# Kernel optimization log

Measured on AMD Instinct MI355X. Metric: run time of the kernel, lower is better.

Reference implementation:

```python
import jax, jax.numpy as jnp
import numpy as np

DIM = 3
LAM = 500.0  # Poisson rate from __init__
LOG2PI = float(np.log(2.0 * np.pi))
JITTER = 1e-6


def setup_inputs() -> dict:
    key = jax.random.key(0)
    ks = jax.random.split(key, 12)
    Lang, A, K, N = 500, 32, 64, 512
    colors = jax.random.normal(ks[0], (Lang, K, DIM), dtype=jnp.float32) * 2.0
    # each alignment is K DISTINCT prototype indices (DPP submatrix must be non-singular)
    u = jax.random.uniform(ks[1], (Lang, A, N))
    alignments = jnp.argsort(u, axis=-1)[..., :K].astype(jnp.int32)
    mus = jax.random.normal(ks[2], (N, DIM), dtype=jnp.float32)
    fk_w1 = jax.random.normal(ks[3], (DIM, DIM), dtype=jnp.float32) * 0.3
    fk_b1 = jax.random.normal(ks[4], (DIM,), dtype=jnp.float32) * 0.1
    fk_w2 = jax.random.normal(ks[5], (1, DIM), dtype=jnp.float32) * 0.3
    fk_b2 = jax.random.normal(ks[6], (1,), dtype=jnp.float32) * 0.1
    df_w1 = jnp.eye(DIM, dtype=jnp.float32) + 0.1 * jax.random.normal(ks[7], (DIM, DIM), dtype=jnp.float32)
    df_b1 = jax.random.normal(ks[8], (DIM,), dtype=jnp.float32) * 0.1
    # last layer initialized to identity in the original module; perturb slightly, keep invertible
    df_w2 = jnp.eye(DIM, dtype=jnp.float32) + 0.05 * jax.random.normal(ks[9], (DIM, DIM), dtype=jnp.float32)
    df_b2 = jax.random.normal(ks[10], (DIM,), dtype=jnp.float32) * 0.1
    return {"colors": colors, "alignments": alignments, "mus": mus,
            "fk_w1": fk_w1, "fk_b1": fk_b1, "fk_w2": fk_w2, "fk_b2": fk_b2,
            "df_w1": df_w1, "df_b1": df_b1, "df_w2": df_w2, "df_b2": df_b2}


def reference(colors, alignments, mus, fk_w1, fk_b1, fk_w2, fk_b2, df_w1, df_b1, df_w2, df_b2):
    N = mus.shape[0]
    K = alignments.shape[-1]

    # step1: Poisson(lambda).log_prob(N)
    Nf = jnp.float32(N)
    step1 = Nf * jnp.log(LAM) - LAM - jax.scipy.special.gammaln(Nf + 1.0)

    # step2: standard MVN prior on prototypes, summed
    step2 = jnp.sum(-0.5 * jnp.sum(mus * mus, axis=-1) - 0.5 * DIM * LOG2PI)

    # L-ensemble: quality (focalization MLP) x RBF diversity
    h = jnp.tanh(mus @ fk_w1.T + fk_b1)            # [N, 3]
    logq = (h @ fk_w2.T + fk_b2)[:, 0]             # [N]
    q = jnp.exp(logq)
    d2 = jnp.sum((mus[:, None, :] - mus[None, :, :]) ** 2, axis=-1)  # [N, N]
    S = jnp.exp(-0.5 * d2)
    L = q[:, None] * S * q[None, :]                # [N, N]
    logdet_LI = jnp.linalg.slogdet(L + jnp.eye(N, dtype=L.dtype))[1]

    # step3: DPP log-prob per alignment: logdet(L_A) - logdet(L + I)
    sub = L[alignments[..., :, None], alignments[..., None, :]]       # [Lang, A, K, K]
    sub = sub + JITTER * jnp.eye(K, dtype=L.dtype)
    step3 = jnp.linalg.slogdet(sub)[1] - logdet_LI                    # [Lang, A]

    # step4: chromes = inverse diffeomorphism of colors (Linear-Tanh-Linear inverted)
    w2_inv = jnp.linalg.inv(df_w2)
    w1_inv = jnp.linalg.inv(df_w1)
    z2 = (colors - df_b2) @ w2_inv.T
    z1 = jnp.arctanh(jnp.clip(z2, -1.0 + 1e-6, 1.0 - 1e-6))
    chromes = (z1 - df_b1) @ w1_inv.T                                 # [Lang, K, 3]

    chromemes = mus[alignments]                                       # [Lang, A, K, 3]
    diff = chromes[:, None, :, :] - chromemes                         # [Lang, A, K, 3]
    step4 = jnp.sum(-0.5 * jnp.sum(diff * diff, axis=-1) - 0.5 * DIM * LOG2PI, axis=-1)  # [Lang, A]

    # per-language logsumexp over alignments, summed over languages
    step34 = jnp.sum(jax.scipy.special.logsumexp(step3 + step4, axis=-1))

    return -(step1 + step2 + step34)
```

## Files before the change

### kernel.cpp

```cpp
#include <hip/hip_runtime.h>
#include <math.h>

#define LOG2PI_F 1.8378770664093453f

#define WS_Q    0
#define WS_SCAL 512
#define WS_M    544
#define WS_CHR  (544 + 512*512)
#define WS_S34  (WS_CHR + 96000)
#define WS_BAR  (WS_S34 + 16000)

#define CHOL_BLOCKS 16

__device__ inline void inv3(const float* w, float* out){
  float a=w[0],b=w[1],c=w[2],d=w[3],e=w[4],f=w[5],g=w[6],h=w[7],i=w[8];
  float A = e*i - f*h;
  float B = -(d*i - f*g);
  float C = d*h - e*g;
  float det = a*A + b*B + c*C;
  float id = 1.0f/det;
  out[0]=A*id;            out[1]=-(b*i - c*h)*id; out[2]=(b*f - c*e)*id;
  out[3]=B*id;            out[4]=(a*i - c*g)*id;  out[5]=-(a*f - c*d)*id;
  out[6]=C*id;            out[7]=-(a*h - b*g)*id; out[8]=(a*e - b*d)*id;
}

__device__ inline void wave_lds_sync(){
  asm volatile("s_waitcnt lgkmcnt(0)" ::: "memory");
}

__device__ inline float rdlane(float v, int l){
  return __int_as_float(__builtin_amdgcn_readlane(__float_as_int(v), l));
}

__device__ inline void gbar(float* ws){
  __syncthreads();
  if (threadIdx.x == 0){
    int* cnt = (int*)(ws + WS_BAR);
    int* gen = (int*)(ws + WS_BAR) + 1;
    int g = __hip_atomic_load(gen, __ATOMIC_RELAXED, __HIP_MEMORY_SCOPE_AGENT);
    int a = __hip_atomic_fetch_add(cnt, 1, __ATOMIC_ACQ_REL, __HIP_MEMORY_SCOPE_AGENT);
    if (a == CHOL_BLOCKS - 1){
      __hip_atomic_store(cnt, 0, __ATOMIC_RELAXED, __HIP_MEMORY_SCOPE_AGENT);
      __hip_atomic_store(gen, g + 1, __ATOMIC_RELEASE, __HIP_MEMORY_SCOPE_AGENT);
    } else {
      while (__hip_atomic_load(gen, __ATOMIC_RELAXED, __HIP_MEMORY_SCOPE_AGENT) == g){
        __builtin_amdgcn_s_sleep(1);
      }
      (void)__hip_atomic_load(gen, __ATOMIC_ACQUIRE, __HIP_MEMORY_SCOPE_AGENT);
    }
  }
  __syncthreads();
}

__global__ __launch_bounds__(512) void k_prep(const float* __restrict__ mus,
    const float* __restrict__ fkw1, const float* __restrict__ fkb1,
    const float* __restrict__ fkw2, const float* __restrict__ fkb2,
    const float* __restrict__ dfw1, const float* __restrict__ dfw2,
    float* ws){
  int t = threadIdx.x;
  __shared__ float red[512];
  float m0 = mus[t*3+0], m1 = mus[t*3+1], m2 = mus[t*3+2];
  float h0 = tanhf(fkw1[0]*m0 + fkw1[1]*m1 + fkw1[2]*m2 + fkb1[0]);
  float h1 = tanhf(fkw1[3]*m0 + fkw1[4]*m1 + fkw1[5]*m2 + fkb1[1]);
  float h2 = tanhf(fkw1[6]*m0 + fkw1[7]*m1 + fkw1[8]*m2 + fkb1[2]);
  float logq = fkw2[0]*h0 + fkw2[1]*h1 + fkw2[2]*h2 + fkb2[0];
  ws[WS_Q + t] = expf(logq);
  red[t] = -0.5f*(m0*m0 + m1*m1 + m2*m2);
  __syncthreads();
  for (int s = 256; s; s >>= 1){ if (t < s) red[t] += red[t+s]; __syncthreads(); }
  if (t == 0){
    ws[WS_SCAL+1] = red[0] - 512.0f*1.5f*LOG2PI_F;
    ws[WS_SCAL+0] = 512.0f*logf(500.0f) - 500.0f - lgammaf(513.0f);
    inv3(dfw1, ws + WS_SCAL + 3);
    inv3(dfw2, ws + WS_SCAL + 12);
    ((int*)(ws + WS_BAR))[0] = 0;
    ((int*)(ws + WS_BAR))[1] = 0;
  }
}

__global__ __launch_bounds__(256) void k_cl(const float* __restrict__ colors,
    const float* __restrict__ dfb1, const float* __restrict__ dfb2,
    const float* __restrict__ mus, float* ws){
  const int b = blockIdx.x;
  if (b < 125){
    int id = b*256 + threadIdx.x;
    const float* w1i = ws + WS_SCAL + 3;
    const float* w2i = ws + WS_SCAL + 12;
    float c0 = colors[id*3+0] - dfb2[0];
    float c1 = colors[id*3+1] - dfb2[1];
    float c2 = colors[id*3+2] - dfb2[2];
    float z0 = w2i[0]*c0 + w2i[1]*c1 + w2i[2]*c2;
    float z1 = w2i[3]*c0 + w2i[4]*c1 + w2i[5]*c2;
    float z2 = w2i[6]*c0 + w2i[7]*c1 + w2i[8]*c2;
    const float lo = -1.0f + 1e-6f, hi = 1.0f - 1e-6f;
    z0 = atanhf(fminf(fmaxf(z0, lo), hi)) - dfb1[0];
    z1 = atanhf(fminf(fmaxf(z1, lo), hi)) - dfb1[1];
    z2 = atanhf(fminf(fmaxf(z2, lo), hi)) - dfb1[2];
    ws[WS_CHR + id*3+0] = w1i[0]*z0 + w1i[1]*z1 + w1i[2]*z2;
    ws[WS_CHR + id*3+1] = w1i[3]*z0 + w1i[4]*z1 + w1i[5]*z2;
    ws[WS_CHR + id*3+2] = w1i[6]*z0 + w1i[7]*z1 + w1i[8]*z2;
  } else {
    int id = (b - 125)*256 + threadIdx.x;
    int i = id >> 9, j = id & 511;
    float dx = mus[i*3+0]-mus[j*3+0];
    float dy = mus[i*3+1]-mus[j*3+1];
    float dz = mus[i*3+2]-mus[j*3+2];
    float d2 = dx*dx + dy*dy + dz*dz;
    float v = ws[WS_Q+i]*ws[WS_Q+j]*expf(-0.5f*d2);
    if (i == j) v += 1.0f;
    ws[WS_M + id] = v;
  }
}

__global__ __launch_bounds__(512) void k_fused(const int* __restrict__ align,
    const float* __restrict__ mus, float* ws){
  __shared__ __align__(16) float smem[16384];

  if (blockIdx.x < CHOL_BLOCKS){
    __builtin_amdgcn_s_setprio(1);
    const int cb = blockIdx.x;
    float* M = ws + WS_M;
    float (*PnT)[512] = reinterpret_cast<float (*)[512]>(smem);
    const int t = threadIdx.x;
    float lgacc = 0.f;

    for (int p = 0; p < 16; ++p){
      const int k0 = p << 5;
      const int H = 512 - k0;
      if (t < H){
        const int r = k0 + t;
        #pragma unroll
        for (int c4 = 0; c4 < 8; ++c4){
          float4 v = *(const float4*)&M[r*512 + k0 + c4*4];
          PnT[c4*4+0][r] = v.x;
          PnT[c4*4+1][r] = v.y;
          PnT[c4*4+2][r] = v.z;
          PnT[c4*4+3][r] = v.w;
        }
      }
      __syncthreads();
      if (t < 32){
        float x[32];
        #pragma unroll
        for (int c = 0; c < 32; ++c) x[c] = PnT[c][k0 + t];
        float invd = 1.f, mydiag = 1.f;
        #pragma unroll
        for (int c = 0; c < 32; ++c){
          float piv = rdlane(x[c], c);
          float sq = sqrtf(fmaxf(piv, 1e-30f));
          float inv = 1.0f / sq;
          float xc = x[c] * inv;
          if (t == c){ xc = sq; invd = inv; mydiag = sq; }
          x[c] = xc;
          #pragma unroll
          for (int j = c + 1; j < 32; ++j){
            float cj = rdlane(x[c], j);
            x[j] -= x[c] * cj;
          }
        }
        #pragma unroll
        for (int c = 0; c < 32; ++c){
          float val = (t > c) ? x[c] : ((t == c) ? invd : 0.f);
          PnT[c][k0 + t] = val;
        }
        float lg = logf(mydiag);
        #pragma unroll
        for (int off = 16; off; off >>= 1) lg += __shfl_down(lg, off);
        if (t == 0) lgacc += lg;
      }
      __syncthreads();
      {
        const int r = k0 + 32 + t;
        if (r < 512){
          float y[32];
          #pragma unroll
          for (int c = 0; c < 32; ++c) y[c] = PnT[c][r];
          #pragma unroll
          for (int c = 0; c < 32; ++c){
            const float inv = PnT[c][k0 + c];
            const float yc = y[c] * inv;
            #pragma unroll
            for (int q4 = c >> 2; q4 < 8; ++q4){
              float4 f = *(const float4*)&PnT[c][k0 + q4*4];
              y[q4*4+0] -= yc * f.x;
              y[q4*4+1] -= yc * f.y;
              y[q4*4+2] -= yc * f.z;
              y[q4*4+3] -= yc * f.w;
            }
            y[c] = yc;
          }
          #pragma unroll
          for (int c = 0; c < 32; ++c) PnT[c][r] = y[c];
        }
      }
      __syncthreads();
      {
        const int T = 480 - k0;
        const int m = (T + 63) >> 6;
        const int P = m * (m + 1) / 2;
        const int h = t >> 8, tt = t & 255, ti = tt >> 4, tj = tt & 15;
        for (int tp = cb*2 + h; tp < P; tp += 2*CHOL_BLOCKS){
          int a = 0;
          while ((a + 1) * (a + 2) / 2 <= tp) a++;
          const int bb = tp - a * (a + 1) / 2;
          const int R  = k0 + 32 + a * 64;
          const int C0 = k0 + 32 + bb * 64;
          const int ra = R + ti * 4, ca = C0 + tj * 4;
          const int ral = ra > 508 ? 508 : ra;
          const int cal = ca > 508 ? 508 : ca;
          float acc[4][4];
          #pragma unroll
          for (int ii = 0; ii < 4; ++ii)
            #pragma unroll
            for (int jj = 0; jj < 4; ++jj) acc[ii][jj] = 0.f;
          #pragma unroll 4
          for (int c = 0; c < 32; ++c){
            float4 av = *(const float4*)&PnT[c][ral];
            float4 bv = *(const float4*)&PnT[c][cal];
            acc[0][0] += av.x*bv.x; acc[0][1] += av.x*bv.y; acc[0][2] += av.x*bv.z; acc[0][3] += av.x*bv.w;
            acc[1][0] += av.y*bv.x; acc[1][1] += av.y*bv.y; acc[1][2] += av.y*bv.z; acc[1][3] += av.y*bv.w;
            acc[2][0] += av.z*bv.x; acc[2][1] += av.z*bv.y; acc[2][2] += av.z*bv.z; acc[2][3] += av.z*bv.w;
            acc[3][0] += av.w*bv.x; acc[3][1] += av.w*bv.y; acc[3][2] += av.w*bv.z; acc[3][3] += av.w*bv.w;
          }
          if (ra < 512 && ca < 512){
            #pragma unroll
            for (int ii = 0; ii < 4; ++ii){
              const int r = ra + ii;
              float4 v = *(float4*)&M[r*512 + ca];
              v.x -= acc[ii][0]; v.y -= acc[ii][1]; v.z -= acc[ii][2]; v.w -= acc[ii][3];
              *(float4*)&M[r*512 + ca] = v;
            }
          }
        }
      }
      if (p < 15) gbar(ws);
    }
    if (cb == 0 && t == 0) ws[WS_SCAL + 2] = 2.f * lgacc;
  } else {
    const int wid = threadIdx.x >> 6;
    const int t   = threadIdx.x & 63;
    const int sp  = ((int)blockIdx.x - CHOL_BLOCKS)*8 + wid;
    float4* pt   = reinterpret_cast<float4*>(smem) + (wid << 6);
    float*  colb = smem + 2048 + (wid << 7);
    const int idx = align[sp*64 + t];
    float4 own;
    own.x = mus[idx*3+0]; own.y = mus[idx*3+1]; own.z = mus[idx*3+2];
    own.w = ws[WS_Q + idx];
    pt[t] = own;
    wave_lds_sync();
    float x[64];
    #pragma unroll
    for (int j = 0; j < 64; ++j){
      float4 o = pt[j];
      float dx = own.x - o.x, dy = own.y - o.y, dz = own.z - o.z;
      float d2 = dx*dx + dy*dy + dz*dz;
      float v = own.w * o.w * expf(-0.5f*d2);
      if (j == t) v += 1e-6f;
      x[j] = v;
    }
    float mydiag = 1.f;
    #pragma unroll
    for (int c = 0; c < 64; ++c){
      float piv = rdlane(x[c], c);
      float sq = sqrtf(fmaxf(piv, 1e-30f));
      float inv = 1.0f / sq;
      float xc = x[c] * inv;
      if (t == c){ xc = sq; mydiag = sq; }
      x[c] = xc;
      float* col = colb + ((c & 1) << 6);
      col[t] = (t > c) ? xc : 0.f;
      wave_lds_sync();
      const int j0 = c + 1;
      const int ja = (j0 + 3) & ~3;
      const int jh = (ja < 64) ? ja : 64;
      #pragma unroll
      for (int j = j0; j < jh; ++j) x[j] -= xc * col[j];
      #pragma unroll
      for (int j = ja; j < 64; j += 4){
        float4 cv = *(const float4*)&col[j];
        x[j+0] -= xc * cv.x;
        x[j+1] -= xc * cv.y;
        x[j+2] -= xc * cv.z;
        x[j+3] -= xc * cv.w;
      }
    }
    const float* ch = ws + WS_CHR + ((sp >> 5)*64 + t)*3;
    float d0 = ch[0] - own.x, d1 = ch[1] - own.y, d2v = ch[2] - own.z;
    float v = 2.f*logf(mydiag) - 0.5f*(d0*d0 + d1*d1 + d2v*d2v);
    #pragma unroll
    for (int off = 32; off; off >>= 1) v += __shfl_down(v, off);
    if (t == 0) ws[WS_S34 + sp] = v - 96.f*LOG2PI_F;
  }
}

__global__ __launch_bounds__(512) void k_final(const float* __restrict__ ws, float* __restrict__ out){
  __shared__ float red[512];
  int t = threadIdx.x;
  float v = 0.f;
  if (t < 500){
    const float* s = ws + WS_S34 + t*32;
    float mx = -1e30f;
    for (int a = 0; a < 32; ++a) mx = fmaxf(mx, s[a]);
    float sum = 0.f;
    for (int a = 0; a < 32; ++a) sum += expf(s[a] - mx);
    v = mx + logf(sum);
  }
  red[t] = v;
  __syncthreads();
  for (int s = 256; s; s >>= 1){ if (t < s) red[t] += red[t+s]; __syncthreads(); }
  if (t == 0){
    float step1 = ws[WS_SCAL+0];
    float step2 = ws[WS_SCAL+1];
    float ld    = ws[WS_SCAL+2];
    float step34 = red[0] - 500.f*ld;
    out[0] = -(step1 + step2 + step34);
  }
}

extern "C" void kernel_launch(void* const* d_in, const int* in_sizes, int n_in,
                              void* d_out, int out_size, void* d_ws, size_t ws_size,
                              hipStream_t stream) {
  const float* colors = (const float*)d_in[0];
  const int*   align  = (const int*)  d_in[1];
  const float* mus    = (const float*)d_in[2];
  const float* fkw1   = (const float*)d_in[3];
  const float* fkb1   = (const float*)d_in[4];
  const float* fkw2   = (const float*)d_in[5];
  const float* fkb2   = (const float*)d_in[6];
  const float* dfw1   = (const float*)d_in[7];
  const float* dfb1   = (const float*)d_in[8];
  const float* dfw2   = (const float*)d_in[9];
  const float* dfb2   = (const float*)d_in[10];
  float* ws  = (float*)d_ws;
  float* out = (float*)d_out;

  hipLaunchKernelGGL(k_prep,  dim3(1),    dim3(512), 0, stream,
                     mus, fkw1, fkb1, fkw2, fkb2, dfw1, dfw2, ws);
  hipLaunchKernelGGL(k_cl,    dim3(1149), dim3(256), 0, stream, colors, dfb1, dfb2, mus, ws);
  hipLaunchKernelGGL(k_fused, dim3(2000 + CHOL_BLOCKS), dim3(512), 0, stream, align, mus, ws);
  hipLaunchKernelGGL(k_final, dim3(1),    dim3(512), 0, stream, ws, out);
}
```

Baseline: 331.9 us.

## Fold final reduction into fused kernel and use lane shuffles in Cholesky

Removes the separate k_final launch by having the last block to finish, detected with an atomic counter, perform the logsumexp and final reduction. The panel Cholesky now runs redundantly in every wave, so the trailing triangular solve reads pivot values through cross-lane reads instead of LDS. This also drops a block barrier. The small 64x64 Cholesky likewise replaces its LDS column broadcast and waitcnt with rdlane broadcasts. This saves a launch and LDS traffic, at the cost of redundant panel work and many more cross-lane read instructions.

```diff
diff --git a/kernel.cpp b/kernel.cpp
--- a/kernel.cpp
+++ b/kernel.cpp
@@ -11,6 +11,8 @@
 #define WS_BAR  (WS_S34 + 16000)
 
 #define CHOL_BLOCKS 16
+#define SMALL_BLOCKS 2000
+#define TOTAL_BLOCKS (CHOL_BLOCKS + SMALL_BLOCKS)
 
 __device__ inline void inv3(const float* w, float* out){
   float a=w[0],b=w[1],c=w[2],d=w[3],e=w[4],f=w[5],g=w[6],h=w[7],i=w[8];
@@ -75,6 +77,7 @@
     inv3(dfw2, ws + WS_SCAL + 12);
     ((int*)(ws + WS_BAR))[0] = 0;
     ((int*)(ws + WS_BAR))[1] = 0;
+    ((int*)(ws + WS_BAR))[2] = 0;
   }
 }
 
@@ -113,8 +116,9 @@
 }
 
 __global__ __launch_bounds__(512) void k_fused(const int* __restrict__ align,
-    const float* __restrict__ mus, float* ws){
+    const float* __restrict__ mus, float* ws, float* __restrict__ out){
   __shared__ __align__(16) float smem[16384];
+  __shared__ int sflag;
 
   if (blockIdx.x < CHOL_BLOCKS){
     __builtin_amdgcn_s_setprio(1);
@@ -139,36 +143,31 @@
         }
       }
       __syncthreads();
+      const int l5 = t & 31;
+      float x[32];
+      #pragma unroll
+      for (int c = 0; c < 32; ++c) x[c] = PnT[c][k0 + l5];
+      float invd = 1.f, mydiag = 1.f;
+      #pragma unroll
+      for (int c = 0; c < 32; ++c){
+        float piv = rdlane(x[c], c);
+        float sq = sqrtf(fmaxf(piv, 1e-30f));
+        float inv = 1.0f / sq;
+        float xc = x[c] * inv;
+        if (l5 == c){ xc = sq; invd = inv; mydiag = sq; }
+        x[c] = xc;
+        #pragma unroll
+        for (int j = c + 1; j < 32; ++j){
+          float cj = rdlane(x[c], j);
+          x[j] -= x[c] * cj;
+        }
+      }
       if (t < 32){
-        float x[32];
-        #pragma unroll
-        for (int c = 0; c < 32; ++c) x[c] = PnT[c][k0 + t];
-        float invd = 1.f, mydiag = 1.f;
-        #pragma unroll
-        for (int c = 0; c < 32; ++c){
-          float piv = rdlane(x[c], c);
-          float sq = sqrtf(fmaxf(piv, 1e-30f));
-          float inv = 1.0f / sq;
-          float xc = x[c] * inv;
-          if (t == c){ xc = sq; invd = inv; mydiag = sq; }
-          x[c] = xc;
-          #pragma unroll
-          for (int j = c + 1; j < 32; ++j){
-            float cj = rdlane(x[c], j);
-            x[j] -= x[c] * cj;
-          }
-        }
-        #pragma unroll
-        for (int c = 0; c < 32; ++c){
-          float val = (t > c) ? x[c] : ((t == c) ? invd : 0.f);
-          PnT[c][k0 + t] = val;
-        }
         float lg = logf(mydiag);
         #pragma unroll
         for (int off = 16; off; off >>= 1) lg += __shfl_down(lg, off);
         if (t == 0) lgacc += lg;
       }
-      __syncthreads();
       {
         const int r = k0 + 32 + t;
         if (r < 512){
@@ -177,15 +176,10 @@
           for (int c = 0; c < 32; ++c) y[c] = PnT[c][r];
           #pragma unroll
           for (int c = 0; c < 32; ++c){
-            const float inv = PnT[c][k0 + c];
-            const float yc = y[c] * inv;
+            const float yc = y[c] * rdlane(invd, c);
             #pragma unroll
-            for (int q4 = c >> 2; q4 < 8; ++q4){
-              float4 f = *(const float4*)&PnT[c][k0 + q4*4];
-              y[q4*4+0] -= yc * f.x;
-              y[q4*4+1] -= yc * f.y;
-              y[q4*4+2] -= yc * f.z;
-              y[q4*4+3] -= yc * f.w;
+            for (int j = c + 1; j < 32; ++j){
+              y[j] -= yc * rdlane(x[c], j);
             }
             y[c] = yc;
           }
@@ -240,8 +234,7 @@
     const int wid = threadIdx.x >> 6;
     const int t   = threadIdx.x & 63;
     const int sp  = ((int)blockIdx.x - CHOL_BLOCKS)*8 + wid;
-    float4* pt   = reinterpret_cast<float4*>(smem) + (wid << 6);
-    float*  colb = smem + 2048 + (wid << 7);
+    float4* pt = reinterpret_cast<float4*>(smem) + (wid << 6);
     const int idx = align[sp*64 + t];
     float4 own;
     own.x = mus[idx*3+0]; own.y = mus[idx*3+1]; own.z = mus[idx*3+2];
@@ -267,21 +260,9 @@
       float xc = x[c] * inv;
       if (t == c){ xc = sq; mydiag = sq; }
       x[c] = xc;
-      float* col = colb + ((c & 1) << 6);
-      col[t] = (t > c) ? xc : 0.f;
-      wave_lds_sync();
-      const int j0 = c + 1;
-      const int ja = (j0 + 3) & ~3;
-      const int jh = (ja < 64) ? ja : 64;
       #pragma unroll
-      for (int j = j0; j < jh; ++j) x[j] -= xc * col[j];
-      #pragma unroll
-      for (int j = ja; j < 64; j += 4){
-        float4 cv = *(const float4*)&col[j];
-        x[j+0] -= xc * cv.x;
-        x[j+1] -= xc * cv.y;
-        x[j+2] -= xc * cv.z;
-        x[j+3] -= xc * cv.w;
+      for (int j = c + 1; j < 64; ++j){
+        x[j] -= xc * rdlane(x[c], j);
       }
     }
     const float* ch = ws + WS_CHR + ((sp >> 5)*64 + t)*3;
@@ -291,29 +272,44 @@
     for (int off = 32; off; off >>= 1) v += __shfl_down(v, off);
     if (t == 0) ws[WS_S34 + sp] = v - 96.f*LOG2PI_F;
   }
-}
-
-__global__ __launch_bounds__(512) void k_final(const float* __restrict__ ws, float* __restrict__ out){
-  __shared__ float red[512];
-  int t = threadIdx.x;
-  float v = 0.f;
-  if (t < 500){
-    const float* s = ws + WS_S34 + t*32;
-    float mx = -1e30f;
-    for (int a = 0; a < 32; ++a) mx = fmaxf(mx, s[a]);
-    float sum = 0.f;
-    for (int a = 0; a < 32; ++a) sum += expf(s[a] - mx);
-    v = mx + logf(sum);
-  }
-  red[t] = v;
-  __syncthreads();
-  for (int s = 256; s; s >>= 1){ if (t < s) red[t] += red[t+s]; __syncthreads(); }
-  if (t == 0){
-    float step1 = ws[WS_SCAL+0];
-    float step2 = ws[WS_SCAL+1];
-    float ld    = ws[WS_SCAL+2];
-    float step34 = red[0] - 500.f*ld;
-    out[0] = -(step1 + step2 + step34);
+
+  __syncthreads();
+  if (threadIdx.x == 0){
+    int* cf = (int*)(ws + WS_BAR) + 2;
+    int a = __hip_atomic_fetch_add(cf, 1, __ATOMIC_ACQ_REL, __HIP_MEMORY_SCOPE_AGENT);
+    int isl = (a == TOTAL_BLOCKS - 1) ? 1 : 0;
+    if (isl) __hip_atomic_store(cf, 0, __ATOMIC_RELAXED, __HIP_MEMORY_SCOPE_AGENT);
+    sflag = isl;
+  }
+  __syncthreads();
+  if (sflag){
+    float* red = smem;
+    const int t = threadIdx.x;
+    float v = 0.f;
+    if (t < 500){
+      const float* s = ws + WS_S34 + t*32;
+      float mx = -1e30f;
+      for (int a = 0; a < 32; ++a) mx = fmaxf(mx, s[a]);
+      float sum = 0.f;
+      for (int a = 0; a < 32; ++a) sum += expf(s[a] - mx);
+      v = mx + logf(sum);
+    }
+    red[t] = v;
+    __syncthreads();
+    for (int s = 256; s; s >>= 1){ if (t < s) red[t] += red[t+s]; __syncthreads(); }
+    float slse = red[0];
+    __syncthreads();
+    float m0 = mus[t*3+0], m1 = mus[t*3+1], m2 = mus[t*3+2];
+    red[t] = -0.5f*(m0*m0 + m1*m1 + m2*m2);
+    __syncthreads();
+    for (int s = 256; s; s >>= 1){ if (t < s) red[t] += red[t+s]; __syncthreads(); }
+    if (t == 0){
+      float step2 = red[0] - 512.0f*1.5f*LOG2PI_F;
+      float step1 = 512.0f*logf(500.0f) - 500.0f - lgammaf(513.0f);
+      float ld    = ws[WS_SCAL + 2];
+      float step34 = slse - 500.f*ld;
+      out[0] = -(step1 + step2 + step34);
+    }
   }
 }
 
@@ -337,6 +333,5 @@
   hipLaunchKernelGGL(k_prep,  dim3(1),    dim3(512), 0, stream,
                      mus, fkw1, fkb1, fkw2, fkb2, dfw1, dfw2, ws);
   hipLaunchKernelGGL(k_cl,    dim3(1149), dim3(256), 0, stream, colors, dfb1, dfb2, mus, ws);
-  hipLaunchKernelGGL(k_fused, dim3(2000 + CHOL_BLOCKS), dim3(512), 0, stream, align, mus, ws);
-  hipLaunchKernelGGL(k_final, dim3(1),    dim3(512), 0, stream, ws, out);
-}
+  hipLaunchKernelGGL(k_fused, dim3(TOTAL_BLOCKS), dim3(512), 0, stream, align, mus, ws, out);
+}
```

New measurement: 379.7 us. 14.4% more time.

## Fuse L-matrix build, chromes and final reduction into the persistent Cholesky kernel

Applied to the files above, without the earlier changes.

Removes the separate k_cl and k_final launches. Cholesky blocks now build their own rows of L+I before the first grid barrier, and the small-block path computes chromes inline from colors. The final logsumexp reduction runs in whichever block arrives last at an atomic counter. The panel triangular solve is spread across all Cholesky blocks through global memory with an extra grid barrier per step, which adds synchronisation cost in exchange for fewer launches and parallel TRSM.

```diff
diff --git a/kernel.cpp b/kernel.cpp
--- a/kernel.cpp
+++ b/kernel.cpp
@@ -6,11 +6,12 @@
 #define WS_Q    0
 #define WS_SCAL 512
 #define WS_M    544
-#define WS_CHR  (544 + 512*512)
-#define WS_S34  (WS_CHR + 96000)
+#define WS_S34  (544 + 512*512)
 #define WS_BAR  (WS_S34 + 16000)
 
 #define CHOL_BLOCKS 16
+#define SMALL_BLOCKS 2000
+#define TOTAL_BLOCKS (CHOL_BLOCKS + SMALL_BLOCKS)
 
 __device__ inline void inv3(const float* w, float* out){
   float a=w[0],b=w[1],c=w[2],d=w[3],e=w[4],f=w[5],g=w[6],h=w[7],i=w[8];
@@ -75,46 +76,16 @@
     inv3(dfw2, ws + WS_SCAL + 12);
     ((int*)(ws + WS_BAR))[0] = 0;
     ((int*)(ws + WS_BAR))[1] = 0;
-  }
-}
-
-__global__ __launch_bounds__(256) void k_cl(const float* __restrict__ colors,
+    ((int*)(ws + WS_BAR))[2] = 0;
+  }
+}
+
+__global__ __launch_bounds__(512) void k_fused(const int* __restrict__ align,
+    const float* __restrict__ mus, const float* __restrict__ colors,
     const float* __restrict__ dfb1, const float* __restrict__ dfb2,
-    const float* __restrict__ mus, float* ws){
-  const int b = blockIdx.x;
-  if (b < 125){
-    int id = b*256 + threadIdx.x;
-    const float* w1i = ws + WS_SCAL + 3;
-    const float* w2i = ws + WS_SCAL + 12;
-    float c0 = colors[id*3+0] - dfb2[0];
-    float c1 = colors[id*3+1] - dfb2[1];
-    float c2 = colors[id*3+2] - dfb2[2];
-    float z0 = w2i[0]*c0 + w2i[1]*c1 + w2i[2]*c2;
-    float z1 = w2i[3]*c0 + w2i[4]*c1 + w2i[5]*c2;
-    float z2 = w2i[6]*c0 + w2i[7]*c1 + w2i[8]*c2;
-    const float lo = -1.0f + 1e-6f, hi = 1.0f - 1e-6f;
-    z0 = atanhf(fminf(fmaxf(z0, lo), hi)) - dfb1[0];
-    z1 = atanhf(fminf(fmaxf(z1, lo), hi)) - dfb1[1];
-    z2 = atanhf(fminf(fmaxf(z2, lo), hi)) - dfb1[2];
-    ws[WS_CHR + id*3+0] = w1i[0]*z0 + w1i[1]*z1 + w1i[2]*z2;
-    ws[WS_CHR + id*3+1] = w1i[3]*z0 + w1i[4]*z1 + w1i[5]*z2;
-    ws[WS_CHR + id*3+2] = w1i[6]*z0 + w1i[7]*z1 + w1i[8]*z2;
-  } else {
-    int id = (b - 125)*256 + threadIdx.x;
-    int i = id >> 9, j = id & 511;
-    float dx = mus[i*3+0]-mus[j*3+0];
-    float dy = mus[i*3+1]-mus[j*3+1];
-    float dz = mus[i*3+2]-mus[j*3+2];
-    float d2 = dx*dx + dy*dy + dz*dz;
-    float v = ws[WS_Q+i]*ws[WS_Q+j]*expf(-0.5f*d2);
-    if (i == j) v += 1.0f;
-    ws[WS_M + id] = v;
-  }
-}
-
-__global__ __launch_bounds__(512) void k_fused(const int* __restrict__ align,
-    const float* __restrict__ mus, float* ws){
+    float* ws, float* __restrict__ out){
   __shared__ __align__(16) float smem[16384];
+  __shared__ int sflag;
 
   if (blockIdx.x < CHOL_BLOCKS){
     __builtin_amdgcn_s_setprio(1);
@@ -124,25 +95,30 @@
     const int t = threadIdx.x;
     float lgacc = 0.f;
 
+    {
+      const float* q = ws + WS_Q;
+      for (int e = t; e < 32*512; e += 512){
+        const int i = (cb << 5) + (e >> 9), j = e & 511;
+        float dx = mus[i*3+0]-mus[j*3+0];
+        float dy = mus[i*3+1]-mus[j*3+1];
+        float dz = mus[i*3+2]-mus[j*3+2];
+        float d2 = dx*dx + dy*dy + dz*dz;
+        float v = q[i]*q[j]*expf(-0.5f*d2);
+        if (i == j) v += 1.0f;
+        M[i*512 + j] = v;
+      }
+    }
+    gbar(ws);
+
     for (int p = 0; p < 16; ++p){
       const int k0 = p << 5;
-      const int H = 512 - k0;
-      if (t < H){
-        const int r = k0 + t;
-        #pragma unroll
-        for (int c4 = 0; c4 < 8; ++c4){
-          float4 v = *(const float4*)&M[r*512 + k0 + c4*4];
-          PnT[c4*4+0][r] = v.x;
-          PnT[c4*4+1][r] = v.y;
-          PnT[c4*4+2][r] = v.z;
-          PnT[c4*4+3][r] = v.w;
-        }
-      }
-      __syncthreads();
       if (t < 32){
         float x[32];
         #pragma unroll
-        for (int c = 0; c < 32; ++c) x[c] = PnT[c][k0 + t];
+        for (int c4 = 0; c4 < 8; ++c4){
+          float4 v = *(const float4*)&M[(k0+t)*512 + k0 + c4*4];
+          x[c4*4+0]=v.x; x[c4*4+1]=v.y; x[c4*4+2]=v.z; x[c4*4+3]=v.w;
+        }
         float invd = 1.f, mydiag = 1.f;
         #pragma unroll
         for (int c = 0; c < 32; ++c){
@@ -169,71 +145,91 @@
         if (t == 0) lgacc += lg;
       }
       __syncthreads();
-      {
-        const int r = k0 + 32 + t;
-        if (r < 512){
-          float y[32];
+      if (p < 15){
+        {
+          const int r = k0 + 32 + t*16 + cb;
+          if (t*16 < 480 - k0 && r < 512){
+            float y[32];
+            #pragma unroll
+            for (int c4 = 0; c4 < 8; ++c4){
+              float4 v = *(const float4*)&M[r*512 + k0 + c4*4];
+              y[c4*4+0]=v.x; y[c4*4+1]=v.y; y[c4*4+2]=v.z; y[c4*4+3]=v.w;
+            }
+            #pragma unroll
+            for (int c = 0; c < 32; ++c){
+              const float inv = PnT[c][k0 + c];
+              const float yc = y[c] * inv;
+              #pragma unroll
+              for (int q4 = c >> 2; q4 < 8; ++q4){
+                float4 f = *(const float4*)&PnT[c][k0 + q4*4];
+                y[q4*4+0] -= yc * f.x;
+                y[q4*4+1] -= yc * f.y;
+                y[q4*4+2] -= yc * f.z;
+                y[q4*4+3] -= yc * f.w;
+              }
+              y[c] = yc;
+            }
+            #pragma unroll
+            for (int c4 = 0; c4 < 8; ++c4){
+              float4 v; v.x=y[c4*4+0]; v.y=y[c4*4+1]; v.z=y[c4*4+2]; v.w=y[c4*4+3];
+              *(float4*)&M[r*512 + k0 + c4*4] = v;
+            }
+          }
+        }
+        gbar(ws);
+        if (t < 480 - k0){
+          const int r = k0 + 32 + t;
           #pragma unroll
-          for (int c = 0; c < 32; ++c) y[c] = PnT[c][r];
-          #pragma unroll
-          for (int c = 0; c < 32; ++c){
-            const float inv = PnT[c][k0 + c];
-            const float yc = y[c] * inv;
+          for (int c4 = 0; c4 < 8; ++c4){
+            float4 v = *(const float4*)&M[r*512 + k0 + c4*4];
+            PnT[c4*4+0][r] = v.x;
+            PnT[c4*4+1][r] = v.y;
+            PnT[c4*4+2][r] = v.z;
+            PnT[c4*4+3][r] = v.w;
+          }
+        }
+        __syncthreads();
+        {
+          const int T = 480 - k0;
+          const int m = (T + 63) >> 6;
+          const int P = m * (m + 1) / 2;
+          const int h = t >> 8, tt = t & 255, ti = tt >> 4, tj = tt & 15;
+          for (int tp = cb*2 + h; tp < P; tp += 2*CHOL_BLOCKS){
+            int a = 0;
+            while ((a + 1) * (a + 2) / 2 <= tp) a++;
+            const int bb = tp - a * (a + 1) / 2;
+            const int R  = k0 + 32 + a * 64;
+            const int C0 = k0 + 32 + bb * 64;
+            const int ra = R + ti * 4, ca = C0 + tj * 4;
+            const int ral = ra > 508 ? 508 : ra;
+            const int cal = ca > 508 ? 508 : ca;
+            float acc[4][4];
             #pragma unroll
-            for (int q4 = c >> 2; q4 < 8; ++q4){
-              float4 f = *(const float4*)&PnT[c][k0 + q4*4];
-              y[q4*4+0] -= yc * f.x;
-              y[q4*4+1] -= yc * f.y;
-              y[q4*4+2] -= yc * f.z;
-              y[q4*4+3] -= yc * f.w;
-            }
-            y[c] = yc;
+            for (int ii = 0; ii < 4; ++ii)
+              #pragma unroll
+              for (int jj = 0; jj < 4; ++jj) acc[ii][jj] = 0.f;
+            #pragma unroll 4
+            for (int c = 0; c < 32; ++c){
+              float4 av = *(const float4*)&PnT[c][ral];
+              float4 bv = *(const float4*)&PnT[c][cal];
+              acc[0][0] += av.x*bv.x; acc[0][1] += av.x*bv.y; acc[0][2] += av.x*bv.z; acc[0][3] += av.x*bv.w;
+              acc[1][0] += av.y*bv.x; acc[1][1] += av.y*bv.y; acc[1][2] += av.y*bv.z; acc[1][3] += av.y*bv.w;
+              acc[2][0] += av.z*bv.x; acc[2][1] += av.z*bv.y; acc[2][2] += av.z*bv.z; acc[2][3] += av.z*bv.w;
+              acc[3][0] += av.w*bv.x; acc[3][1] += av.w*bv.y; acc[3][2] += av.w*bv.z; acc[3][3] += av.w*bv.w;
+            }
+            if (ra < 512 && ca < 512){
+              #pragma unroll
+              for (int ii = 0; ii < 4; ++ii){
+                const int r = ra + ii;
+                float4 v = *(float4*)&M[r*512 + ca];
+                v.x -= acc[ii][0]; v.y -= acc[ii][1]; v.z -= acc[ii][2]; v.w -= acc[ii][3];
+                *(float4*)&M[r*512 + ca] = v;
+              }
+            }
           }
-          #pragma unroll
-          for (int c = 0; c < 32; ++c) PnT[c][r] = y[c];
-        }
-      }
-      __syncthreads();
-      {
-        const int T = 480 - k0;
-        const int m = (T + 63) >> 6;
-        const int P = m * (m + 1) / 2;
-        const int h = t >> 8, tt = t & 255, ti = tt >> 4, tj = tt & 15;
-        for (int tp = cb*2 + h; tp < P; tp += 2*CHOL_BLOCKS){
-          int a = 0;
-          while ((a + 1) * (a + 2) / 2 <= tp) a++;
-          const int bb = tp - a * (a + 1) / 2;
-          const int R  = k0 + 32 + a * 64;
-          const int C0 = k0 + 32 + bb * 64;
-          const int ra = R + ti * 4, ca = C0 + tj * 4;
-          const int ral = ra > 508 ? 508 : ra;
-          const int cal = ca > 508 ? 508 : ca;
-          float acc[4][4];
-          #pragma unroll
-          for (int ii = 0; ii < 4; ++ii)
-            #pragma unroll
-            for (int jj = 0; jj < 4; ++jj) acc[ii][jj] = 0.f;
-          #pragma unroll 4
-          for (int c = 0; c < 32; ++c){
-            float4 av = *(const float4*)&PnT[c][ral];
-            float4 bv = *(const float4*)&PnT[c][cal];
-            acc[0][0] += av.x*bv.x; acc[0][1] += av.x*bv.y; acc[0][2] += av.x*bv.z; acc[0][3] += av.x*bv.w;
-            acc[1][0] += av.y*bv.x; acc[1][1] += av.y*bv.y; acc[1][2] += av.y*bv.z; acc[1][3] += av.y*bv.w;
-            acc[2][0] += av.z*bv.x; acc[2][1] += av.z*bv.y; acc[2][2] += av.z*bv.z; acc[2][3] += av.z*bv.w;
-            acc[3][0] += av.w*bv.x; acc[3][1] += av.w*bv.y; acc[3][2] += av.w*bv.z; acc[3][3] += av.w*bv.w;
-          }
-          if (ra < 512 && ca < 512){
-            #pragma unroll
-            for (int ii = 0; ii < 4; ++ii){
-              const int r = ra + ii;
-              float4 v = *(float4*)&M[r*512 + ca];
-              v.x -= acc[ii][0]; v.y -= acc[ii][1]; v.z -= acc[ii][2]; v.w -= acc[ii][3];
-              *(float4*)&M[r*512 + ca] = v;
-            }
-          }
-        }
-      }
-      if (p < 15) gbar(ws);
+        }
+        gbar(ws);
+      }
     }
     if (cb == 0 && t == 0) ws[WS_SCAL + 2] = 2.f * lgacc;
   } else {
@@ -284,36 +280,66 @@
         x[j+3] -= xc * cv.w;
       }
     }
-    const float* ch = ws + WS_CHR + ((sp >> 5)*64 + t)*3;
-    float d0 = ch[0] - own.x, d1 = ch[1] - own.y, d2v = ch[2] - own.z;
+    const int cid = ((sp >> 5) << 6) + t;
+    const float* w1i = ws + WS_SCAL + 3;
+    const float* w2i = ws + WS_SCAL + 12;
+    float c0 = colors[cid*3+0] - dfb2[0];
+    float c1 = colors[cid*3+1] - dfb2[1];
+    float c2 = colors[cid*3+2] - dfb2[2];
+    float z0 = w2i[0]*c0 + w2i[1]*c1 + w2i[2]*c2;
+    float z1 = w2i[3]*c0 + w2i[4]*c1 + w2i[5]*c2;
+    float z2 = w2i[6]*c0 + w2i[7]*c1 + w2i[8]*c2;
+    const float lo = -1.0f + 1e-6f, hi = 1.0f - 1e-6f;
+    z0 = atanhf(fminf(fmaxf(z0, lo), hi)) - dfb1[0];
+    z1 = atanhf(fminf(fmaxf(z1, lo), hi)) - dfb1[1];
+    z2 = atanhf(fminf(fmaxf(z2, lo), hi)) - dfb1[2];
+    float ch0 = w1i[0]*z0 + w1i[1]*z1 + w1i[2]*z2;
+    float ch1 = w1i[3]*z0 + w1i[4]*z1 + w1i[5]*z2;
+    float ch2 = w1i[6]*z0 + w1i[7]*z1 + w1i[8]*z2;
+    float d0 = ch0 - own.x, d1 = ch1 - own.y, d2v = ch2 - own.z;
     float v = 2.f*logf(mydiag) - 0.5f*(d0*d0 + d1*d1 + d2v*d2v);
     #pragma unroll
     for (int off = 32; off; off >>= 1) v += __shfl_down(v, off);
     if (t == 0) ws[WS_S34 + sp] = v - 96.f*LOG2PI_F;
   }
-}
-
-__global__ __launch_bounds__(512) void k_final(const float* __restrict__ ws, float* __restrict__ out){
-  __shared__ float red[512];
-  int t = threadIdx.x;
-  float v = 0.f;
-  if (t < 500){
-    const float* s = ws + WS_S34 + t*32;
-    float mx = -1e30f;
-    for (int a = 0; a < 32; ++a) mx = fmaxf(mx, s[a]);
-    float sum = 0.f;
-    for (int a = 0; a < 32; ++a) sum += expf(s[a] - mx);
-    v = mx + logf(sum);
-  }
-  red[t] = v;
-  __syncthreads();
-  for (int s = 256; s; s >>= 1){ if (t < s) red[t] += red[t+s]; __syncthreads(); }
-  if (t == 0){
-    float step1 = ws[WS_SCAL+0];
-    float step2 = ws[WS_SCAL+1];
-    float ld    = ws[WS_SCAL+2];
-    float step34 = red[0] - 500.f*ld;
-    out[0] = -(step1 + step2 + step34);
+
+  __syncthreads();
+  if (threadIdx.x == 0){
+    int* cf = (int*)(ws + WS_BAR) + 2;
+    int a = __hip_atomic_fetch_add(cf, 1, __ATOMIC_ACQ_REL, __HIP_MEMORY_SCOPE_AGENT);
+    int isl = (a == TOTAL_BLOCKS - 1) ? 1 : 0;
+    if (isl) __hip_atomic_store(cf, 0, __ATOMIC_RELAXED, __HIP_MEMORY_SCOPE_AGENT);
+    sflag = isl;
+  }
+  __syncthreads();
+  if (sflag){
+    float* red = smem;
+    const int t = threadIdx.x;
+    float v = 0.f;
+    if (t < 500){
+      const float* s = ws + WS_S34 + t*32;
+      float mx = -1e30f;
+      for (int a = 0; a < 32; ++a) mx = fmaxf(mx, s[a]);
+      float sum = 0.f;
+      for (int a = 0; a < 32; ++a) sum += expf(s[a] - mx);
+      v = mx + logf(sum);
+    }
+    red[t] = v;
+    __syncthreads();
+    for (int s = 256; s; s >>= 1){ if (t < s) red[t] += red[t+s]; __syncthreads(); }
+    float slse = red[0];
+    __syncthreads();
+    float m0 = mus[t*3+0], m1 = mus[t*3+1], m2 = mus[t*3+2];
+    red[t] = -0.5f*(m0*m0 + m1*m1 + m2*m2);
+    __syncthreads();
+    for (int s = 256; s; s >>= 1){ if (t < s) red[t] += red[t+s]; __syncthreads(); }
+    if (t == 0){
+      float step2 = red[0] - 512.0f*1.5f*LOG2PI_F;
+      float step1 = 512.0f*logf(500.0f) - 500.0f - lgammaf(513.0f);
+      float ld    = ws[WS_SCAL + 2];
+      float step34 = slse - 500.f*ld;
+      out[0] = -(step1 + step2 + step34);
+    }
   }
 }
 
@@ -334,9 +360,8 @@
   float* ws  = (float*)d_ws;
   float* out = (float*)d_out;
 
-  hipLaunchKernelGGL(k_prep,  dim3(1),    dim3(512), 0, stream,
+  hipLaunchKernelGGL(k_prep,  dim3(1), dim3(512), 0, stream,
                      mus, fkw1, fkb1, fkw2, fkb2, dfw1, dfw2, ws);
-  hipLaunchKernelGGL(k_cl,    dim3(1149), dim3(256), 0, stream, colors, dfb1, dfb2, mus, ws);
-  hipLaunchKernelGGL(k_fused, dim3(2000 + CHOL_BLOCKS), dim3(512), 0, stream, align, mus, ws);
-  hipLaunchKernelGGL(k_final, dim3(1),    dim3(512), 0, stream, ws, out);
-}
+  hipLaunchKernelGGL(k_fused, dim3(TOTAL_BLOCKS), dim3(512), 0, stream,
+                     align, mus, colors, dfb1, dfb2, ws, out);
+}
```

After: 547.6 us. 65.0% more time.
